# Optimization experiments

Hardware: AMD Instinct MI355X
Metric: run time of the kernel (lower is better)

## Reference

```python
import jax, jax.numpy as jnp
import numpy as np

B, P, K = 2, 8192, 20
ELL = 0.15          # ell_min + ell_rand
ELL_BASE = 10.0     # ell_basedist
COLOR_SCALE = 0.2
RES_MIN = 0.1       # res_mag_min
RES_MAX = 2.0       # res_mag_max
BIG = 1e10          # masking constant for invalid db points
EPS = 1e-12


def setup_inputs() -> dict:
    key = jax.random.key(0)
    ks = jax.random.split(key, 16)
    scale = jnp.array([20.0, 20.0, 60.0], jnp.float32)
    off = jnp.array([-10.0, -10.0, 1.0], jnp.float32)  # depth z in [1, 61] m
    xyz1 = jax.random.uniform(ks[0], (B, P, 3), jnp.float32) * scale + off
    xyz2 = jax.random.uniform(ks[1], (B, P, 3), jnp.float32) * scale + off
    hsv1 = jax.random.uniform(ks[2], (B, P, 3), jnp.float32)
    hsv2 = jax.random.uniform(ks[3], (B, P, 3), jnp.float32)
    n1 = jax.random.normal(ks[4], (B, P, 3), jnp.float32)
    normal1 = n1 / jnp.linalg.norm(n1, axis=-1, keepdims=True)
    n2 = jax.random.normal(ks[5], (B, P, 3), jnp.float32)
    normal2 = n2 / jnp.linalg.norm(n2, axis=-1, keepdims=True)
    nres1 = jax.random.uniform(ks[6], (B, P, 1), jnp.float32)
    nres2 = jax.random.uniform(ks[7], (B, P, 1), jnp.float32)

    def rot(k):
        a = np.asarray(jax.random.normal(k, (B, 3, 3), jnp.float32))
        q, _ = np.linalg.qr(a)
        return jnp.asarray(q, jnp.float32)

    R12 = rot(ks[8])
    R21 = rot(ks[9])
    t12 = jax.random.normal(ks[10], (B, 3, 1), jnp.float32) * 0.5
    t21 = jax.random.normal(ks[11], (B, 3, 1), jnp.float32) * 0.5
    npts1 = jax.random.randint(ks[12], (B,), P // 2, P + 1)
    npts2 = jax.random.randint(ks[13], (B,), P // 2, P + 1)
    return dict(xyz1=xyz1, xyz2=xyz2, hsv1=hsv1, hsv2=hsv2,
                normal1=normal1, normal2=normal2, nres1=nres1, nres2=nres2,
                R12=R12, t12=t12, R21=R21, t21=t21, npts1=npts1, npts2=npts2)


def _knn(pq, pdb, len_db):
    # pq [B,Pq,3], pdb [B,Pdb,3] -> squared dists [B,Pq,K], idx [B,Pq,K]
    d2 = jnp.sum((pq[:, :, None, :] - pdb[:, None, :, :]) ** 2, axis=-1)
    valid = jnp.arange(pdb.shape[1])[None, :] < len_db[:, None]
    d2 = jnp.where(valid[:, None, :], d2, BIG)
    neg, idx = jax.lax.top_k(-d2, K)
    return -neg, idx


def _gather(f, idx):
    # f [B,Pdb,C], idx [B,Pq,K] -> [B,Pq,K,C]  (knn_gather)
    return jax.vmap(lambda fb, ib: fb[ib])(f, idx)


def _transform(xyz, normal, R, t):
    x = jnp.einsum('bij,bpj->bpi', R, xyz) + t[:, :, 0][:, None, :]
    n = jnp.einsum('bij,bpj->bpi', R, normal)
    return x, n


def _side(pq, hq, nq, rq, lq, pdb, hdb, ndb, rdb, ldb):
    dists, idx = _knn(pq, pdb, ldb)                      # [B,P,K]
    # length_scale = clamp(ell*(z-base)/base, min=ell)^2
    ls = jnp.maximum(ELL * (pq[:, :, 2:3] - ELL_BASE) / ELL_BASE, ELL) ** 2
    dist_k = jnp.exp(-dists / ls)
    hsv_knn = _gather(hdb, idx)                          # [B,P,K,3]
    cdist = jnp.sqrt(jnp.sum((hq[:, :, None, :] - hsv_knn) ** 2, -1) + EPS)
    color_k = jnp.exp(-cdist / COLOR_SCALE)
    n_knn = _gather(ndb, idx)                            # [B,P,K,3]
    r_knn = _gather(rdb, idx)                            # [B,P,K,1]
    alpha = (2 * RES_MIN / (2 * RES_MIN / RES_MAX + rq[:, :, None, :] + r_knn))[..., 0]
    normal_k = jnp.maximum(jnp.sum(nq[:, :, None, :] * n_knn, -1) * alpha, 0.0)
    mask = (jnp.arange(pq.shape[1])[None, :, None] < lq[:, None, None]).astype(dist_k.dtype)
    total = jnp.sum(dist_k * color_k * normal_k * mask)
    return total / (lq.sum().astype(dist_k.dtype) * K)


def reference(xyz1, xyz2, hsv1, hsv2, normal1, normal2, nres1, nres2,
              R12, t12, R21, t21, npts1, npts2):
    x2in1, n2in1 = _transform(xyz2, normal2, R12, t12)   # pcl_gt_2_in_1
    x1in2, n1in2 = _transform(xyz1, normal1, R21, t21)   # pcl_gt_1_in_2
    k1 = _side(xyz1, hsv1, normal1, nres1, npts1, x2in1, hsv2, n2in1, nres2, npts2)
    k2 = _side(xyz2, hsv2, normal2, nres2, npts2, x1in2, hsv1, n1in2, nres1, npts1)
    return (k1 + k2) / 2
```

## Files before the change

### kernel.cpp

```cpp
#include <hip/hip_runtime.h>
#include <cstdint>
#include <cstddef>

#define PBUF 8192
#define NZB 256
#define NYB 32
#define NBINS (NZB * NYB)
#define NCOMBO 4
#define KNN 20
#define CAP 256

#define ZMIN_F (-72.0f)
#define BINW (144.0f / 256.0f)
#define INV_BINW (256.0f / 144.0f)
#define YBINW (144.0f / 32.0f)
#define INV_YBINW (32.0f / 144.0f)

#define IDX_MASK 0x1FFFu
#define D2_MASK 0xFFFFE000u
#define KEY_INF 0xFFFFFFFFu

#define THR_MULT 21.0f

#define OFF_ACCUM   0
#define OFF_DBSTART 2048
#define OFF_DBCUR   (OFF_DBSTART + NCOMBO * (NBINS + 1) * 4)
#define OFF_DBPOS   (OFF_DBCUR + NCOMBO * NBINS * 4)
#define ARR_BYTES   (NCOMBO * PBUF * 16)
#define OFF_DBF1    (OFF_DBPOS + ARR_BYTES)
#define OFF_DBF2    (OFF_DBF1 + ARR_BYTES)

__device__ __forceinline__ int binOfZ(float z) {
  int b = (int)floorf((z - ZMIN_F) * INV_BINW);
  return min(max(b, 0), NZB - 1);
}
__device__ __forceinline__ int binOfY(float y) {
  int b = (int)floorf((y - ZMIN_F) * INV_YBINW);
  return min(max(b, 0), NYB - 1);
}

__device__ __forceinline__ float xformRow(const float* R, float tr, float x0, float x1, float x2) {
  return __fmaf_rn(R[2], x2, __fmaf_rn(R[1], x1, __fmaf_rn(R[0], x0, tr)));
}

__global__ void k_count(const float* xyz1, const float* xyz2,
                        const float* R12, const float* t12,
                        const float* R21, const float* t21,
                        const int* npts1, const int* npts2, char* ws) {
  int tid = blockIdx.x * 256 + threadIdx.x;
  int c = tid >> 13, j = tid & (PBUF - 1);
  int s = c >> 1, b = c & 1;
  const float* dsrc = s == 0 ? xyz2 : xyz1;
  const float* R  = (s == 0 ? R12 : R21) + b * 9;
  const float* tt = (s == 0 ? t12 : t21) + b * 3;
  int ldb = (s == 0 ? npts2 : npts1)[b];
  if (j < ldb) {
    const float* x = dsrc + (size_t)(b * PBUF + j) * 3;
    float y1 = xformRow(R + 3, tt[1], x[0], x[1], x[2]);
    float y2 = xformRow(R + 6, tt[2], x[0], x[1], x[2]);
    int bin = binOfZ(y2) * NYB + binOfY(y1);
    atomicAdd((int*)(ws + OFF_DBCUR) + c * NBINS + bin, 1);
  }
}

__global__ void k_prefix(char* ws) {
  __shared__ int sTot[256];
  const int c = blockIdx.x;
  const int t = threadIdx.x;
  int* cnt = (int*)(ws + OFF_DBCUR) + c * NBINS;
  int* st  = (int*)(ws + OFF_DBSTART) + c * (NBINS + 1);
  int vals[32];
  int base = t * 32;
  int sum = 0;
  #pragma unroll
  for (int k = 0; k < 32; ++k) { vals[k] = cnt[base + k]; sum += vals[k]; }
  sTot[t] = sum;
  __syncthreads();
  for (int o = 1; o < 256; o <<= 1) {
    int v = (t >= o) ? sTot[t - o] : 0;
    __syncthreads();
    sTot[t] += v;
    __syncthreads();
  }
  int run = sTot[t] - sum;
  #pragma unroll
  for (int k = 0; k < 32; ++k) {
    st[base + k] = run;
    cnt[base + k] = run;
    run += vals[k];
  }
  if (t == 255) st[NBINS] = run;
}

__global__ void k_scatter(const float* xyz1, const float* xyz2,
                          const float* hsv1, const float* hsv2,
                          const float* normal1, const float* normal2,
                          const float* nres1, const float* nres2,
                          const float* R12, const float* t12,
                          const float* R21, const float* t21,
                          const int* npts1, const int* npts2, char* ws) {
  int tid = blockIdx.x * 256 + threadIdx.x;
  int c = tid >> 13, j = tid & (PBUF - 1);
  int s = c >> 1, b = c & 1;
  size_t pj = (size_t)(b * PBUF + j);

  const float* dsrc = s == 0 ? xyz2 : xyz1;
  const float* dh = s == 0 ? hsv2 : hsv1;
  const float* dn = s == 0 ? normal2 : normal1;
  const float* dr = s == 0 ? nres2 : nres1;
  const float* R  = (s == 0 ? R12 : R21) + b * 9;
  const float* tt = (s == 0 ? t12 : t21) + b * 3;
  int ldb = (s == 0 ? npts2 : npts1)[b];
  if (j < ldb) {
    const float* x = dsrc + pj * 3;
    float y0 = xformRow(R + 0, tt[0], x[0], x[1], x[2]);
    float y1 = xformRow(R + 3, tt[1], x[0], x[1], x[2]);
    float y2 = xformRow(R + 6, tt[2], x[0], x[1], x[2]);
    const float* n = dn + pj * 3;
    float n0 = xformRow(R + 0, 0.f, n[0], n[1], n[2]);
    float n1 = xformRow(R + 3, 0.f, n[0], n[1], n[2]);
    float n2 = xformRow(R + 6, 0.f, n[0], n[1], n[2]);
    const float* h = dh + pj * 3;
    float r = dr[pj];
    int bin = binOfZ(y2) * NYB + binOfY(y1);
    int pos = atomicAdd((int*)(ws + OFF_DBCUR) + c * NBINS + bin, 1) + c * PBUF;
    ((float4*)(ws + OFF_DBPOS))[pos] = make_float4(y0, y1, y2, 0.f);
    ((float4*)(ws + OFF_DBF1))[pos] = make_float4(h[0], h[1], h[2], r);
    ((float4*)(ws + OFF_DBF2))[pos] = make_float4(n0, n1, n2, 0.f);
  }
}

__global__ __launch_bounds__(256) void k_main(
    const float* xyz1, const float* xyz2,
    const float* hsv1, const float* hsv2,
    const float* normal1, const float* normal2,
    const float* nres1, const float* nres2,
    const int* npts1, const int* npts2, char* ws) {
  __shared__ unsigned sBuf[4 * CAP];
  const int lane = threadIdx.x & 63;
  const int wIn = threadIdx.x >> 6;
  const int gw = blockIdx.x * 4 + wIn;
  const int c = gw >> 13;
  const int qi = (int)(__brev((unsigned)(gw & 8191)) >> 19);
  const int s = c >> 1, b = c & 1;
  const int lq = (s == 0 ? npts1 : npts2)[b];
  if (qi >= lq) return;

  const size_t qo = (size_t)(b * PBUF + qi);
  const float* qx = (s == 0 ? xyz1 : xyz2) + qo * 3;
  const float* qh = (s == 0 ? hsv1 : hsv2) + qo * 3;
  const float* qn = (s == 0 ? normal1 : normal2) + qo * 3;
  const float* qr = (s == 0 ? nres1 : nres2) + qo;
  const float qpx = qx[0], qpy = qx[1], qpz = qx[2];
  const float qh0 = qh[0], qh1 = qh[1], qh2 = qh[2];
  const float qn0 = qn[0], qn1 = qn[1], qn2 = qn[2];
  const float qres = qr[0];

  const float ell = fmaxf(0.015f * (qpz - 10.0f), 0.15f);
  const float ls = ell * ell;
  const float thrF = THR_MULT * ls;
  const float rad = sqrtf(thrF);

  const int* F = (const int*)(ws + OFF_DBSTART) + c * (NBINS + 1);
  const int zlo = binOfZ(qpz - rad), zhi = binOfZ(qpz + rad);
  const int ylo = binOfY(qpy - rad), yhi = binOfY(qpy + rad);
  const int nseg = zhi - zlo + 1;

  int segS = 0, segLen = 0;
  if (lane < nseg) {
    int zk = zlo + lane;
    segS = F[zk * NYB + ylo];
    segLen = F[zk * NYB + yhi + 1] - segS;
  }
  int cum = segLen;
  #pragma unroll
  for (int o = 1; o < 64; o <<= 1) {
    int n = __shfl_up(cum, o);
    if (lane >= o) cum += n;
  }
  const int L = __shfl(cum, 63);
  const int excl = cum - segLen;

  const float4* dbPos = (const float4*)(ws + OFF_DBPOS) + c * PBUF;
  const float4* dbF1  = (const float4*)(ws + OFF_DBF1) + c * PBUF;
  const float4* dbF2  = (const float4*)(ws + OFF_DBF2) + c * PBUF;

  unsigned* buf = sBuf + wIn * CAP;
  int pos = 0;
  for (int base = 0; base < L; base += 64) {
    int t = base + lane;
    bool in = t < L;
    int tc = min(t, L - 1);
    int kk = 0;
    #pragma unroll
    for (int step = 8; step; step >>= 1) {
      int cnd = kk + step;
      int e = __shfl(excl, cnd & 63);
      if (cnd < nseg && e <= tc) kk = cnd;
    }
    int j = __shfl(segS, kk) + (tc - __shfl(excl, kk));
    float4 p = dbPos[j];
    float dx = p.x - qpx, dy = p.y - qpy, dz = p.z - qpz;
    float d2 = __fmaf_rn(dx, dx, __fmaf_rn(dy, dy, dz * dz));
    bool keep = in && (d2 <= thrF);
    unsigned long long m = __ballot(keep);
    int rank = (int)__popcll(m & ((1ull << lane) - 1ull));
    if (keep) {
      int pidx = pos + rank;
      if (pidx < CAP) buf[pidx] = (__float_as_uint(d2) & D2_MASK) | (unsigned)j;
    }
    pos += (int)__popcll(m);
  }
  pos = min(pos, CAP);

  unsigned key = KEY_INF;
  if (pos <= KNN) {
    if (lane < pos) key = buf[lane];
  } else if (pos <= 64) {
    unsigned v = (lane < pos) ? buf[lane] : KEY_INF;
    #pragma unroll
    for (int k = 2; k <= 64; k <<= 1) {
      #pragma unroll
      for (int j2 = k >> 1; j2 > 0; j2 >>= 1) {
        unsigned o = __shfl_xor(v, j2);
        bool up = (lane & k) == 0;
        bool lowhalf = (lane & j2) == 0;
        v = (lowhalf == up) ? min(v, o) : max(v, o);
      }
    }
    key = v;
  } else {
    unsigned r0 = (lane < pos) ? buf[lane] : KEY_INF;
    unsigned r1 = (lane + 64 < pos) ? buf[lane + 64] : KEY_INF;
    unsigned r2 = (lane + 128 < pos) ? buf[lane + 128] : KEY_INF;
    unsigned r3 = (lane + 192 < pos) ? buf[lane + 192] : KEY_INF;
    { unsigned lo, hi;
      lo = min(r0, r1); hi = max(r0, r1); r0 = lo; r1 = hi;
      lo = min(r2, r3); hi = max(r2, r3); r2 = lo; r3 = hi;
      lo = min(r0, r2); hi = max(r0, r2); r0 = lo; r2 = hi;
      lo = min(r1, r3); hi = max(r1, r3); r1 = lo; r3 = hi;
      lo = min(r1, r2); hi = max(r1, r2); r1 = lo; r2 = hi; }
    unsigned kout = KEY_INF;
    #pragma unroll
    for (int t = 0; t < KNN; ++t) {
      unsigned m0 = r0;
      m0 = min(m0, __shfl_xor(m0, 1));
      m0 = min(m0, __shfl_xor(m0, 2));
      m0 = min(m0, __shfl_xor(m0, 4));
      m0 = min(m0, __shfl_xor(m0, 8));
      m0 = min(m0, __shfl_xor(m0, 16));
      m0 = min(m0, __shfl_xor(m0, 32));
      unsigned long long bal = __ballot(r0 == m0);
      int owner = __ffsll(bal) - 1;
      if (lane == owner) { r0 = r1; r1 = r2; r2 = r3; r3 = KEY_INF; }
      if (lane == t) kout = m0;
    }
    key = kout;
  }

  float lsum = 0.f;
  if (lane < KNN && key != KEY_INF) {
    int j = (int)(key & IDX_MASK);
    float4 p = dbPos[j];
    float4 f1 = dbF1[j];
    float4 f2 = dbF2[j];
    float dx = p.x - qpx, dy = p.y - qpy, dz = p.z - qpz;
    float d2 = __fmaf_rn(dx, dx, __fmaf_rn(dy, dy, dz * dz));
    float inv_ls = 1.0f / ls;
    float dist_k = __expf(-d2 * inv_ls);
    float c0 = qh0 - f1.x, c1 = qh1 - f1.y, c2 = qh2 - f1.z;
    float cd = sqrtf(__fmaf_rn(c0, c0, __fmaf_rn(c1, c1, c2 * c2)) + 1e-12f);
    float color_k = __expf(cd * -5.0f);
    float alpha = 0.2f / (0.1f + qres + f1.w);
    float nd = __fmaf_rn(qn0, f2.x, __fmaf_rn(qn1, f2.y, qn2 * f2.z));
    float nk = fmaxf(nd * alpha, 0.0f);
    lsum = dist_k * color_k * nk;
  }
  #pragma unroll
  for (int o = 32; o; o >>= 1) lsum += __shfl_down(lsum, o);
  if (lane == 0)
    atomicAdd((float*)(ws + OFF_ACCUM) + (s * 256 + (blockIdx.x & 255)), lsum);
}

__global__ void k_final(const int* npts1, const int* npts2, const char* ws, float* out) {
  int lane = threadIdx.x;
  const float* acc = (const float*)(ws + OFF_ACCUM);
  float s1 = acc[lane] + acc[lane + 64] + acc[lane + 128] + acc[lane + 192];
  float s2 = acc[256 + lane] + acc[256 + lane + 64] + acc[256 + lane + 128] + acc[256 + lane + 192];
  #pragma unroll
  for (int o = 32; o; o >>= 1) {
    s1 += __shfl_down(s1, o);
    s2 += __shfl_down(s2, o);
  }
  if (lane == 0) {
    float k1 = s1 / (20.0f * (float)(npts1[0] + npts1[1]));
    float k2 = s2 / (20.0f * (float)(npts2[0] + npts2[1]));
    out[0] = 0.5f * (k1 + k2);
  }
}

extern "C" void kernel_launch(void* const* d_in, const int* in_sizes, int n_in,
                              void* d_out, int out_size, void* d_ws, size_t ws_size,
                              hipStream_t stream) {
  const float* xyz1 = (const float*)d_in[0];
  const float* xyz2 = (const float*)d_in[1];
  const float* hsv1 = (const float*)d_in[2];
  const float* hsv2 = (const float*)d_in[3];
  const float* normal1 = (const float*)d_in[4];
  const float* normal2 = (const float*)d_in[5];
  const float* nres1 = (const float*)d_in[6];
  const float* nres2 = (const float*)d_in[7];
  const float* R12 = (const float*)d_in[8];
  const float* t12 = (const float*)d_in[9];
  const float* R21 = (const float*)d_in[10];
  const float* t21 = (const float*)d_in[11];
  const int* npts1 = (const int*)d_in[12];
  const int* npts2 = (const int*)d_in[13];
  char* ws = (char*)d_ws;
  float* out = (float*)d_out;

  hipMemsetAsync(ws, 0, OFF_DBPOS, stream);
  k_count<<<dim3(NCOMBO * PBUF / 256), dim3(256), 0, stream>>>(
      xyz1, xyz2, R12, t12, R21, t21, npts1, npts2, ws);
  k_prefix<<<dim3(NCOMBO), dim3(256), 0, stream>>>(ws);
  k_scatter<<<dim3(NCOMBO * PBUF / 256), dim3(256), 0, stream>>>(
      xyz1, xyz2, hsv1, hsv2, normal1, normal2, nres1, nres2,
      R12, t12, R21, t21, npts1, npts2, ws);
  k_main<<<dim3(NCOMBO * PBUF / 4), dim3(256), 0, stream>>>(
      xyz1, xyz2, hsv1, hsv2, normal1, normal2, nres1, nres2, npts1, npts2, ws);
  k_final<<<dim3(1), dim3(64), 0, stream>>>(npts1, npts2, ws, out);
}
```

Measured before the change: 135.9 us.

## Fuse count/prefix into one LDS-histogram kernel, rank-based top-K, last-block final reduce

Merges the bin-count and prefix-scan kernels into a single per-combo kernel that builds the histogram in shared memory and zeroes the accumulators itself, which drops the memset and one launch. Replaces the bitonic and iterative shuffle-min top-K selection with a rank-counting pass over the candidate buffer, so each lane evaluates up to four keys whose rank is below K. Folds the final reduction into k_main using a done-counter so the last block writes the output, removing another launch. The count kernel now runs on only 4 blocks with serial loops over 8192 points, and the rank count costs O(pos) per lane for every query, which may cost more than it saves when candidate lists are long.

```diff
diff --git a/kernel.cpp b/kernel.cpp
--- a/kernel.cpp
+++ b/kernel.cpp
@@ -11,9 +11,7 @@
 #define CAP 256
 
 #define ZMIN_F (-72.0f)
-#define BINW (144.0f / 256.0f)
 #define INV_BINW (256.0f / 144.0f)
-#define YBINW (144.0f / 32.0f)
 #define INV_YBINW (32.0f / 144.0f)
 
 #define IDX_MASK 0x1FFFu
@@ -23,7 +21,8 @@
 #define THR_MULT 21.0f
 
 #define OFF_ACCUM   0
-#define OFF_DBSTART 2048
+#define OFF_DONE    2048
+#define OFF_DBSTART 2064
 #define OFF_DBCUR   (OFF_DBSTART + NCOMBO * (NBINS + 1) * 4)
 #define OFF_DBPOS   (OFF_DBCUR + NCOMBO * NBINS * 4)
 #define ARR_BYTES   (NCOMBO * PBUF * 16)
@@ -43,37 +42,46 @@
   return __fmaf_rn(R[2], x2, __fmaf_rn(R[1], x1, __fmaf_rn(R[0], x0, tr)));
 }
 
-__global__ void k_count(const float* xyz1, const float* xyz2,
-                        const float* R12, const float* t12,
-                        const float* R21, const float* t21,
-                        const int* npts1, const int* npts2, char* ws) {
-  int tid = blockIdx.x * 256 + threadIdx.x;
-  int c = tid >> 13, j = tid & (PBUF - 1);
-  int s = c >> 1, b = c & 1;
+__global__ __launch_bounds__(256) void k_cp(
+    const float* xyz1, const float* xyz2,
+    const float* R12, const float* t12,
+    const float* R21, const float* t21,
+    const int* npts1, const int* npts2, char* ws) {
+  __shared__ int hist[NBINS];
+  __shared__ int sTot[256];
+  const int c = blockIdx.x, t = threadIdx.x;
+  const int s = c >> 1, b = c & 1;
+
+  #pragma unroll
+  for (int k = 0; k < 32; ++k) hist[t + 256 * k] = 0;
+  if (c == 0) {
+    int* z = (int*)ws;
+    for (int i = t; i < 516; i += 256) z[i] = 0;
+  }
+  __syncthreads();
+
   const float* dsrc = s == 0 ? xyz2 : xyz1;
   const float* R  = (s == 0 ? R12 : R21) + b * 9;
   const float* tt = (s == 0 ? t12 : t21) + b * 3;
-  int ldb = (s == 0 ? npts2 : npts1)[b];
-  if (j < ldb) {
-    const float* x = dsrc + (size_t)(b * PBUF + j) * 3;
-    float y1 = xformRow(R + 3, tt[1], x[0], x[1], x[2]);
-    float y2 = xformRow(R + 6, tt[2], x[0], x[1], x[2]);
-    int bin = binOfZ(y2) * NYB + binOfY(y1);
-    atomicAdd((int*)(ws + OFF_DBCUR) + c * NBINS + bin, 1);
-  }
-}
-
-__global__ void k_prefix(char* ws) {
-  __shared__ int sTot[256];
-  const int c = blockIdx.x;
-  const int t = threadIdx.x;
-  int* cnt = (int*)(ws + OFF_DBCUR) + c * NBINS;
-  int* st  = (int*)(ws + OFF_DBSTART) + c * (NBINS + 1);
+  const int ldb = (s == 0 ? npts2 : npts1)[b];
+
+  for (int j = t; j < PBUF; j += 256) {
+    if (j < ldb) {
+      const float* x = dsrc + (size_t)(b * PBUF + j) * 3;
+      float x0 = x[0], x1 = x[1], x2 = x[2];
+      float y1 = xformRow(R + 3, tt[1], x0, x1, x2);
+      float y2 = xformRow(R + 6, tt[2], x0, x1, x2);
+      int bin = binOfZ(y2) * NYB + binOfY(y1);
+      atomicAdd(&hist[bin], 1);
+    }
+  }
+  __syncthreads();
+
   int vals[32];
   int base = t * 32;
   int sum = 0;
   #pragma unroll
-  for (int k = 0; k < 32; ++k) { vals[k] = cnt[base + k]; sum += vals[k]; }
+  for (int k = 0; k < 32; ++k) { vals[k] = hist[base + k]; sum += vals[k]; }
   sTot[t] = sum;
   __syncthreads();
   for (int o = 1; o < 256; o <<= 1) {
@@ -83,6 +91,8 @@
     __syncthreads();
   }
   int run = sTot[t] - sum;
+  int* st  = (int*)(ws + OFF_DBSTART) + c * (NBINS + 1);
+  int* cnt = (int*)(ws + OFF_DBCUR) + c * NBINS;
   #pragma unroll
   for (int k = 0; k < 32; ++k) {
     st[base + k] = run;
@@ -135,8 +145,9 @@
     const float* hsv1, const float* hsv2,
     const float* normal1, const float* normal2,
     const float* nres1, const float* nres2,
-    const int* npts1, const int* npts2, char* ws) {
-  __shared__ unsigned sBuf[4 * CAP];
+    const int* npts1, const int* npts2, char* ws, float* out) {
+  __shared__ unsigned sBuf[4 * (CAP + 4)];
+  __shared__ bool sLast;
   const int lane = threadIdx.x & 63;
   const int wIn = threadIdx.x >> 6;
   const int gw = blockIdx.x * 4 + wIn;
@@ -144,158 +155,141 @@
   const int qi = (int)(__brev((unsigned)(gw & 8191)) >> 19);
   const int s = c >> 1, b = c & 1;
   const int lq = (s == 0 ? npts1 : npts2)[b];
-  if (qi >= lq) return;
-
-  const size_t qo = (size_t)(b * PBUF + qi);
-  const float* qx = (s == 0 ? xyz1 : xyz2) + qo * 3;
-  const float* qh = (s == 0 ? hsv1 : hsv2) + qo * 3;
-  const float* qn = (s == 0 ? normal1 : normal2) + qo * 3;
-  const float* qr = (s == 0 ? nres1 : nres2) + qo;
-  const float qpx = qx[0], qpy = qx[1], qpz = qx[2];
-  const float qh0 = qh[0], qh1 = qh[1], qh2 = qh[2];
-  const float qn0 = qn[0], qn1 = qn[1], qn2 = qn[2];
-  const float qres = qr[0];
-
-  const float ell = fmaxf(0.015f * (qpz - 10.0f), 0.15f);
-  const float ls = ell * ell;
-  const float thrF = THR_MULT * ls;
-  const float rad = sqrtf(thrF);
-
-  const int* F = (const int*)(ws + OFF_DBSTART) + c * (NBINS + 1);
-  const int zlo = binOfZ(qpz - rad), zhi = binOfZ(qpz + rad);
-  const int ylo = binOfY(qpy - rad), yhi = binOfY(qpy + rad);
-  const int nseg = zhi - zlo + 1;
-
-  int segS = 0, segLen = 0;
-  if (lane < nseg) {
-    int zk = zlo + lane;
-    segS = F[zk * NYB + ylo];
-    segLen = F[zk * NYB + yhi + 1] - segS;
-  }
-  int cum = segLen;
-  #pragma unroll
-  for (int o = 1; o < 64; o <<= 1) {
-    int n = __shfl_up(cum, o);
-    if (lane >= o) cum += n;
-  }
-  const int L = __shfl(cum, 63);
-  const int excl = cum - segLen;
-
-  const float4* dbPos = (const float4*)(ws + OFF_DBPOS) + c * PBUF;
-  const float4* dbF1  = (const float4*)(ws + OFF_DBF1) + c * PBUF;
-  const float4* dbF2  = (const float4*)(ws + OFF_DBF2) + c * PBUF;
-
-  unsigned* buf = sBuf + wIn * CAP;
-  int pos = 0;
-  for (int base = 0; base < L; base += 64) {
-    int t = base + lane;
-    bool in = t < L;
-    int tc = min(t, L - 1);
-    int kk = 0;
+
+  if (qi < lq) {
+    const size_t qo = (size_t)(b * PBUF + qi);
+    const float* qx = (s == 0 ? xyz1 : xyz2) + qo * 3;
+    const float* qh = (s == 0 ? hsv1 : hsv2) + qo * 3;
+    const float* qn = (s == 0 ? normal1 : normal2) + qo * 3;
+    const float* qr = (s == 0 ? nres1 : nres2) + qo;
+    const float qpx = qx[0], qpy = qx[1], qpz = qx[2];
+    const float qh0 = qh[0], qh1 = qh[1], qh2 = qh[2];
+    const float qn0 = qn[0], qn1 = qn[1], qn2 = qn[2];
+    const float qres = qr[0];
+
+    const float ell = fmaxf(0.015f * (qpz - 10.0f), 0.15f);
+    const float ls = ell * ell;
+    const float thrF = THR_MULT * ls;
+    const float rad = sqrtf(thrF);
+    const float inv_ls = 1.0f / ls;
+
+    const int* F = (const int*)(ws + OFF_DBSTART) + c * (NBINS + 1);
+    const int zlo = binOfZ(qpz - rad), zhi = binOfZ(qpz + rad);
+    const int ylo = binOfY(qpy - rad), yhi = binOfY(qpy + rad);
+    const int nseg = zhi - zlo + 1;
+
+    int segS = 0, segLen = 0;
+    if (lane < nseg) {
+      int zk = zlo + lane;
+      segS = F[zk * NYB + ylo];
+      segLen = F[zk * NYB + yhi + 1] - segS;
+    }
+    int cum = segLen;
     #pragma unroll
-    for (int step = 8; step; step >>= 1) {
-      int cnd = kk + step;
-      int e = __shfl(excl, cnd & 63);
-      if (cnd < nseg && e <= tc) kk = cnd;
-    }
-    int j = __shfl(segS, kk) + (tc - __shfl(excl, kk));
-    float4 p = dbPos[j];
-    float dx = p.x - qpx, dy = p.y - qpy, dz = p.z - qpz;
-    float d2 = __fmaf_rn(dx, dx, __fmaf_rn(dy, dy, dz * dz));
-    bool keep = in && (d2 <= thrF);
-    unsigned long long m = __ballot(keep);
-    int rank = (int)__popcll(m & ((1ull << lane) - 1ull));
-    if (keep) {
-      int pidx = pos + rank;
-      if (pidx < CAP) buf[pidx] = (__float_as_uint(d2) & D2_MASK) | (unsigned)j;
-    }
-    pos += (int)__popcll(m);
-  }
-  pos = min(pos, CAP);
-
-  unsigned key = KEY_INF;
-  if (pos <= KNN) {
-    if (lane < pos) key = buf[lane];
-  } else if (pos <= 64) {
-    unsigned v = (lane < pos) ? buf[lane] : KEY_INF;
-    #pragma unroll
-    for (int k = 2; k <= 64; k <<= 1) {
+    for (int o = 1; o < 64; o <<= 1) {
+      int n = __shfl_up(cum, o);
+      if (lane >= o) cum += n;
+    }
+    const int L = __shfl(cum, 63);
+    const int excl = cum - segLen;
+
+    const float4* dbPos = (const float4*)(ws + OFF_DBPOS) + c * PBUF;
+    const float4* dbF1  = (const float4*)(ws + OFF_DBF1) + c * PBUF;
+    const float4* dbF2  = (const float4*)(ws + OFF_DBF2) + c * PBUF;
+
+    unsigned* buf = sBuf + wIn * (CAP + 4);
+    int pos = 0;
+    for (int base = 0; base < L; base += 64) {
+      int t = base + lane;
+      bool in = t < L;
+      int tc = min(t, L - 1);
+      int kk = 0;
       #pragma unroll
-      for (int j2 = k >> 1; j2 > 0; j2 >>= 1) {
-        unsigned o = __shfl_xor(v, j2);
-        bool up = (lane & k) == 0;
-        bool lowhalf = (lane & j2) == 0;
-        v = (lowhalf == up) ? min(v, o) : max(v, o);
+      for (int step = 8; step; step >>= 1) {
+        int cnd = kk + step;
+        int e = __shfl(excl, cnd & 63);
+        if (cnd < nseg && e <= tc) kk = cnd;
       }
-    }
-    key = v;
-  } else {
-    unsigned r0 = (lane < pos) ? buf[lane] : KEY_INF;
-    unsigned r1 = (lane + 64 < pos) ? buf[lane + 64] : KEY_INF;
+      int j = __shfl(segS, kk) + (tc - __shfl(excl, kk));
+      float4 p = dbPos[j];
+      float dx = p.x - qpx, dy = p.y - qpy, dz = p.z - qpz;
+      float d2 = __fmaf_rn(dx, dx, __fmaf_rn(dy, dy, dz * dz));
+      bool keep = in && (d2 <= thrF);
+      unsigned long long m = __ballot(keep);
+      int rank = (int)__popcll(m & ((1ull << lane) - 1ull));
+      if (keep) {
+        int pidx = pos + rank;
+        if (pidx < CAP) buf[pidx] = (__float_as_uint(d2) & D2_MASK) | (unsigned)j;
+      }
+      pos += (int)__popcll(m);
+    }
+    pos = min(pos, CAP);
+
+    if (lane < 4) buf[pos + lane] = KEY_INF;
+    unsigned r0 = (lane       < pos) ? buf[lane]       : KEY_INF;
+    unsigned r1 = (lane + 64  < pos) ? buf[lane + 64]  : KEY_INF;
     unsigned r2 = (lane + 128 < pos) ? buf[lane + 128] : KEY_INF;
     unsigned r3 = (lane + 192 < pos) ? buf[lane + 192] : KEY_INF;
-    { unsigned lo, hi;
-      lo = min(r0, r1); hi = max(r0, r1); r0 = lo; r1 = hi;
-      lo = min(r2, r3); hi = max(r2, r3); r2 = lo; r3 = hi;
-      lo = min(r0, r2); hi = max(r0, r2); r0 = lo; r2 = hi;
-      lo = min(r1, r3); hi = max(r1, r3); r1 = lo; r3 = hi;
-      lo = min(r1, r2); hi = max(r1, r2); r1 = lo; r2 = hi; }
-    unsigned kout = KEY_INF;
+    int k0 = 0, k1 = 0, k2 = 0, k3 = 0;
+    const int nch = (pos + 3) >> 2;
+    const uint4* b4 = (const uint4*)buf;
+    for (int ch = 0; ch < nch; ++ch) {
+      uint4 q4 = b4[ch];
+      k0 += (q4.x < r0) + (q4.y < r0) + (q4.z < r0) + (q4.w < r0);
+      k1 += (q4.x < r1) + (q4.y < r1) + (q4.z < r1) + (q4.w < r1);
+      k2 += (q4.x < r2) + (q4.y < r2) + (q4.z < r2) + (q4.w < r2);
+      k3 += (q4.x < r3) + (q4.y < r3) + (q4.z < r3) + (q4.w < r3);
+    }
+
+    auto evalKey = [&](unsigned key, int rk) -> float {
+      if (rk >= KNN || key == KEY_INF) return 0.f;
+      int j = (int)(key & IDX_MASK);
+      float4 p = dbPos[j];
+      float4 f1 = dbF1[j];
+      float4 f2 = dbF2[j];
+      float dx = p.x - qpx, dy = p.y - qpy, dz = p.z - qpz;
+      float d2 = __fmaf_rn(dx, dx, __fmaf_rn(dy, dy, dz * dz));
+      float dist_k = __expf(-d2 * inv_ls);
+      float c0 = qh0 - f1.x, c1 = qh1 - f1.y, c2 = qh2 - f1.z;
+      float cd = sqrtf(__fmaf_rn(c0, c0, __fmaf_rn(c1, c1, c2 * c2)) + 1e-12f);
+      float color_k = __expf(cd * -5.0f);
+      float alpha = 0.2f / (0.1f + qres + f1.w);
+      float nd = __fmaf_rn(qn0, f2.x, __fmaf_rn(qn1, f2.y, qn2 * f2.z));
+      float nk = fmaxf(nd * alpha, 0.0f);
+      return dist_k * color_k * nk;
+    };
+    float lsum = evalKey(r0, k0) + evalKey(r1, k1) + evalKey(r2, k2) + evalKey(r3, k3);
+
     #pragma unroll
-    for (int t = 0; t < KNN; ++t) {
-      unsigned m0 = r0;
-      m0 = min(m0, __shfl_xor(m0, 1));
-      m0 = min(m0, __shfl_xor(m0, 2));
-      m0 = min(m0, __shfl_xor(m0, 4));
-      m0 = min(m0, __shfl_xor(m0, 8));
-      m0 = min(m0, __shfl_xor(m0, 16));
-      m0 = min(m0, __shfl_xor(m0, 32));
-      unsigned long long bal = __ballot(r0 == m0);
-      int owner = __ffsll(bal) - 1;
-      if (lane == owner) { r0 = r1; r1 = r2; r2 = r3; r3 = KEY_INF; }
-      if (lane == t) kout = m0;
-    }
-    key = kout;
-  }
-
-  float lsum = 0.f;
-  if (lane < KNN && key != KEY_INF) {
-    int j = (int)(key & IDX_MASK);
-    float4 p = dbPos[j];
-    float4 f1 = dbF1[j];
-    float4 f2 = dbF2[j];
-    float dx = p.x - qpx, dy = p.y - qpy, dz = p.z - qpz;
-    float d2 = __fmaf_rn(dx, dx, __fmaf_rn(dy, dy, dz * dz));
-    float inv_ls = 1.0f / ls;
-    float dist_k = __expf(-d2 * inv_ls);
-    float c0 = qh0 - f1.x, c1 = qh1 - f1.y, c2 = qh2 - f1.z;
-    float cd = sqrtf(__fmaf_rn(c0, c0, __fmaf_rn(c1, c1, c2 * c2)) + 1e-12f);
-    float color_k = __expf(cd * -5.0f);
-    float alpha = 0.2f / (0.1f + qres + f1.w);
-    float nd = __fmaf_rn(qn0, f2.x, __fmaf_rn(qn1, f2.y, qn2 * f2.z));
-    float nk = fmaxf(nd * alpha, 0.0f);
-    lsum = dist_k * color_k * nk;
-  }
-  #pragma unroll
-  for (int o = 32; o; o >>= 1) lsum += __shfl_down(lsum, o);
-  if (lane == 0)
-    atomicAdd((float*)(ws + OFF_ACCUM) + (s * 256 + (blockIdx.x & 255)), lsum);
-}
-
-__global__ void k_final(const int* npts1, const int* npts2, const char* ws, float* out) {
-  int lane = threadIdx.x;
-  const float* acc = (const float*)(ws + OFF_ACCUM);
-  float s1 = acc[lane] + acc[lane + 64] + acc[lane + 128] + acc[lane + 192];
-  float s2 = acc[256 + lane] + acc[256 + lane + 64] + acc[256 + lane + 128] + acc[256 + lane + 192];
-  #pragma unroll
-  for (int o = 32; o; o >>= 1) {
-    s1 += __shfl_down(s1, o);
-    s2 += __shfl_down(s2, o);
-  }
-  if (lane == 0) {
-    float k1 = s1 / (20.0f * (float)(npts1[0] + npts1[1]));
-    float k2 = s2 / (20.0f * (float)(npts2[0] + npts2[1]));
-    out[0] = 0.5f * (k1 + k2);
+    for (int o = 32; o; o >>= 1) lsum += __shfl_down(lsum, o);
+    if (lane == 0)
+      atomicAdd((float*)(ws + OFF_ACCUM) + (s * 256 + (blockIdx.x & 255)), lsum);
+  }
+
+  __syncthreads();
+  if (threadIdx.x == 0) {
+    __threadfence();
+    sLast = atomicAdd((unsigned*)(ws + OFF_DONE), 1u) == (unsigned)(gridDim.x - 1);
+  }
+  __syncthreads();
+  if (sLast && threadIdx.x < 64) {
+    float* acc = (float*)(ws + OFF_ACCUM);
+    float s1 = 0.f, s2 = 0.f;
+    #pragma unroll
+    for (int i = 0; i < 4; ++i) {
+      s1 += atomicAdd(acc + (threadIdx.x + 64 * i), 0.0f);
+      s2 += atomicAdd(acc + (256 + threadIdx.x + 64 * i), 0.0f);
+    }
+    #pragma unroll
+    for (int o = 32; o; o >>= 1) {
+      s1 += __shfl_down(s1, o);
+      s2 += __shfl_down(s2, o);
+    }
+    if (threadIdx.x == 0) {
+      float k1 = s1 / (20.0f * (float)(npts1[0] + npts1[1]));
+      float k2 = s2 / (20.0f * (float)(npts2[0] + npts2[1]));
+      out[0] = 0.5f * (k1 + k2);
+    }
   }
 }
 
@@ -319,14 +313,11 @@
   char* ws = (char*)d_ws;
   float* out = (float*)d_out;
 
-  hipMemsetAsync(ws, 0, OFF_DBPOS, stream);
-  k_count<<<dim3(NCOMBO * PBUF / 256), dim3(256), 0, stream>>>(
+  k_cp<<<dim3(NCOMBO), dim3(256), 0, stream>>>(
       xyz1, xyz2, R12, t12, R21, t21, npts1, npts2, ws);
-  k_prefix<<<dim3(NCOMBO), dim3(256), 0, stream>>>(ws);
   k_scatter<<<dim3(NCOMBO * PBUF / 256), dim3(256), 0, stream>>>(
       xyz1, xyz2, hsv1, hsv2, normal1, normal2, nres1, nres2,
       R12, t12, R21, t21, npts1, npts2, ws);
   k_main<<<dim3(NCOMBO * PBUF / 4), dim3(256), 0, stream>>>(
-      xyz1, xyz2, hsv1, hsv2, normal1, normal2, nres1, nres2, npts1, npts2, ws);
-  k_final<<<dim3(1), dim3(64), 0, stream>>>(npts1, npts2, ws, out);
-}
+      xyz1, xyz2, hsv1, hsv2, normal1, normal2, nres1, nres2, npts1, npts2, ws, out);
+}
```

New measurement: 260.0 us. +91.3%, slower.
